# Optimization experiments

Measured on AMD Instinct MI355X. Metric: run time of the kernel, lower is better.

## Reference

```python
import jax, jax.numpy as jnp
import numpy as np
from jax import lax

N = 1024          # n_ligand == n_receptor == feature dim (required by broadcast in source)
D = 1024          # gnn_input_dim == gnn_output_dim
H = 32            # hopi_output_dim
C = 32            # cnn_channels


def setup_inputs() -> dict:
    key = jax.random.key(0)
    ks = jax.random.split(key, 24)
    s = 0.02
    inp = {
        "ligand_node_features": jax.random.normal(ks[0], (N, D), jnp.float32),
        "ligand_edge_features": jax.random.normal(ks[1], (N, D), jnp.float32),
        "ligand_adjacency": jax.random.uniform(ks[2], (N, N), jnp.float32),
        "receptor_node_features": jax.random.normal(ks[3], (N, D), jnp.float32),
        "receptor_edge_features": jax.random.normal(ks[4], (N, D), jnp.float32),
        "receptor_adjacency": jax.random.uniform(ks[5], (N, N), jnp.float32),
        # GNNLayer params (shared between ligand and receptor, as in source)
        "Wn": jax.random.normal(ks[6], (D, D), jnp.float32) * s,
        "bn": jax.random.normal(ks[7], (D,), jnp.float32) * s,
        "We": jax.random.normal(ks[8], (D, D), jnp.float32) * s,
        "be": jax.random.normal(ks[9], (D,), jnp.float32) * s,
        "Wa": jax.random.normal(ks[10], (1, D), jnp.float32) * s,
        "ba": jax.random.normal(ks[11], (1,), jnp.float32) * s,
        # HighOrderPairwiseInteraction: Linear(2*D -> H)
        "W_hopi": jax.random.normal(ks[12], (H, 2 * D), jnp.float32) * s,
        "b_hopi": jax.random.normal(ks[13], (H,), jnp.float32) * s,
        # CNN tail
        "conv1_w": jax.random.normal(ks[14], (C, H, 3, 3), jnp.float32) * s,
        "conv1_b": jax.random.normal(ks[15], (C,), jnp.float32) * s,
        "conv2_w": jax.random.normal(ks[16], (C, C, 3, 3), jnp.float32) * s,
        "conv2_b": jax.random.normal(ks[17], (C,), jnp.float32) * s,
        "conv3_w": jax.random.normal(ks[18], (1, C, 1, 1), jnp.float32) * s,
        "conv3_b": jax.random.normal(ks[19], (1,), jnp.float32) * s,
    }
    return inp


def _gnn(nf, ef, Wn, bn, We, be, Wa, ba):
    # aggregated: [N, D]
    agg = jnp.tanh(nf @ Wn.T + bn + ef @ We.T + be)
    scores = agg @ Wa.T + ba                      # [N, 1]
    attn = jax.nn.softmax(scores, axis=1)         # softmax over size-1 dim -> ones (faithful)
    weighted = jnp.sum(agg * attn, axis=1)        # [N]
    return nf + weighted                          # [N,D] + [N] broadcasts over last dim (D == N)


def _conv(x, w, b):
    y = lax.conv_general_dilated(x, w, (1, 1), "SAME",
                                 dimension_numbers=("NCHW", "OIHW", "NCHW"))
    return y + b[None, :, None, None]


def reference(ligand_node_features, ligand_edge_features, ligand_adjacency,
              receptor_node_features, receptor_edge_features, receptor_adjacency,
              Wn, bn, We, be, Wa, ba, W_hopi, b_hopi,
              conv1_w, conv1_b, conv2_w, conv2_b, conv3_w, conv3_b):
    lig = _gnn(ligand_node_features, ligand_edge_features, Wn, bn, We, be, Wa, ba)
    rec = _gnn(receptor_node_features, receptor_edge_features, Wn, bn, We, be, Wa, ba)

    # HOPI: interactions[i, j] = Linear(cat(lig[i], rec[j])) == lig[i] @ Wl.T + rec[j] @ Wr.T + b
    Wl, Wr = W_hopi[:, :D], W_hopi[:, D:]
    lig_p = lig @ Wl.T                            # [N, H]
    rec_p = rec @ Wr.T                            # [N, H]
    interactions = lig_p[:, None, :] + rec_p[None, :, :] + b_hopi  # [N, N, H]

    x = jnp.transpose(interactions, (2, 0, 1))[None]  # [1, H, N, N]
    x = jax.nn.relu(_conv(x, conv1_w, conv1_b))
    x = jax.nn.relu(_conv(x, conv2_w, conv2_b))
    x = _conv(x, conv3_w, conv3_b)                # [1, 1, N, N]
    return x[0, 0]                                # [N, N]
```

## Files before the change

### kernel.cpp

```cpp
#include <hip/hip_runtime.h>


typedef _Float16 half8 __attribute__((ext_vector_type(8)));
typedef _Float16 half4 __attribute__((ext_vector_type(4)));
typedef float    f32x4 __attribute__((ext_vector_type(4)));

__device__ __forceinline__ short f2h_bits(float f){
    _Float16 h = (_Float16)f;
    return __builtin_bit_cast(short, h);
}
__device__ __forceinline__ half8 pack2(const float4& x, const float4& y){
    half8 r;
    r[0] = (_Float16)x.x; r[1] = (_Float16)x.y;
    r[2] = (_Float16)x.z; r[3] = (_Float16)x.w;
    r[4] = (_Float16)y.x; r[5] = (_Float16)y.y;
    r[6] = (_Float16)y.z; r[7] = (_Float16)y.w;
    return r;
}
__device__ __forceinline__ half4 pack4(const float4& x){
    half4 r;
    r[0] = (_Float16)x.x; r[1] = (_Float16)x.y;
    r[2] = (_Float16)x.z; r[3] = (_Float16)x.w;
    return r;
}
__device__ __forceinline__ float tanh_fast(float x){
    float e = __expf(2.f * x);
    return 1.f - 2.f / (e + 1.f);
}

#define SWZ(c) ((((c) >> 1) & 3) << 3)

#define GNN_LOAD(AV, BV, KBN) {                                              \
    const int kbn_ = (KBN) & 2047;                                           \
    const float* Asrc_ = (kbn_ < 1024) ? A0 : A1;                            \
    const float* Bsrc_ = (kbn_ < 1024) ? Wn : We;                            \
    const int kk_ = kbn_ & 1023;                                             \
    const float* ap_ = Asrc_ + (size_t)(j0 + arow) * 1024 + kk_ + akc;       \
    const float* bp_ = Bsrc_ + (size_t)(d0 + brow) * 1024 + kk_ + bkc;       \
    AV[0] = *reinterpret_cast<const float4*>(ap_);                           \
    AV[1] = *reinterpret_cast<const float4*>(ap_ + 4);                       \
    AV[2] = *reinterpret_cast<const float4*>(ap_ + 8);                       \
    AV[3] = *reinterpret_cast<const float4*>(ap_ + 12);                      \
    BV[0] = *reinterpret_cast<const float4*>(bp_);                           \
    BV[1] = *reinterpret_cast<const float4*>(bp_ + 4);                       \
}

#define GNN_STAGE(AV, BV) {                                                  \
    const int ga_ = (t & 3) * 2;                                             \
    const int sa_ = arow & 7;                                                \
    *reinterpret_cast<half8*>(&As[arow * 64 + ((ga_    ) ^ sa_) * 8]) = pack2(AV[0], AV[1]); \
    *reinterpret_cast<half8*>(&As[arow * 64 + ((ga_ + 1) ^ sa_) * 8]) = pack2(AV[2], AV[3]); \
    *reinterpret_cast<half8*>(&Bs[brow * 64 + ((t & 7) ^ (brow & 7)) * 8]) = pack2(BV[0], BV[1]); \
}

#define GNN_MFMA() {                                                         \
    _Pragma("unroll")                                                        \
    for (int ks = 0; ks < 2; ++ks){                                          \
        half8 Af[2], Bf[2];                                                  \
        _Pragma("unroll")                                                    \
        for (int m = 0; m < 2; ++m){                                         \
            int row = wm * 32 + m * 16 + lr;                                 \
            int g   = ((ks * 4 + lg) ^ (row & 7)) * 8;                       \
            Af[m] = *reinterpret_cast<const half8*>(&As[row * 64 + g]);      \
        }                                                                    \
        _Pragma("unroll")                                                    \
        for (int n = 0; n < 2; ++n){                                         \
            int col = wn * 32 + n * 16 + lr;                                 \
            int g   = ((ks * 4 + lg) ^ (col & 7)) * 8;                       \
            Bf[n] = *reinterpret_cast<const half8*>(&Bs[col * 64 + g]);      \
        }                                                                    \
        _Pragma("unroll")                                                    \
        for (int m = 0; m < 2; ++m)                                          \
            _Pragma("unroll")                                                \
            for (int n = 0; n < 2; ++n)                                      \
                acc[m][n] = __builtin_amdgcn_mfma_f32_16x16x32_f16(          \
                    Af[m], Bf[n], acc[m][n], 0, 0, 0);                       \
    }                                                                        \
}

__global__ __launch_bounds__(512) void gnn_kernel(
    const float* __restrict__ lig_nf, const float* __restrict__ lig_ef,
    const float* __restrict__ rec_nf, const float* __restrict__ rec_ef,
    const float* __restrict__ Wn, const float* __restrict__ We,
    const float* __restrict__ bn, const float* __restrict__ be,
    float* __restrict__ part)
{
    __shared__ __attribute__((aligned(16))) short As[128 * 64];
    __shared__ __attribute__((aligned(16))) short Bs[64 * 64];
    __shared__ float red[128][2];

    const int t  = threadIdx.x;
    const int cx = blockIdx.z;
    const float* A0 = cx ? rec_nf : lig_nf;
    const float* A1 = cx ? rec_ef : lig_ef;
    const int j0 = blockIdx.x * 128;
    const int d0 = blockIdx.y * 64;

    const int wid  = t >> 6;
    const int wm   = wid >> 1;
    const int wn   = wid & 1;
    const int lane = t & 63;
    const int lr   = lane & 15;
    const int lg   = lane >> 4;

    f32x4 acc[2][2];
    #pragma unroll
    for (int m = 0; m < 2; ++m)
        #pragma unroll
        for (int n = 0; n < 2; ++n)
            acc[m][n] = (f32x4){0.f, 0.f, 0.f, 0.f};

    const int arow = t >> 2;
    const int akc  = (t & 3) * 16;
    const int brow = t >> 3;
    const int bkc  = (t & 7) * 8;

    float4 avA[4], bvA[2], avB[4], bvB[2];
    GNN_LOAD(avA, bvA, 0);
    GNN_LOAD(avB, bvB, 64);

    for (int kb = 0; kb < 2048; kb += 128){
        __syncthreads();
        GNN_STAGE(avA, bvA);
        GNN_LOAD(avA, bvA, kb + 128);
        __syncthreads();
        GNN_MFMA();
        __syncthreads();
        GNN_STAGE(avB, bvB);
        GNN_LOAD(avB, bvB, kb + 192);
        __syncthreads();
        GNN_MFMA();
    }

    float rowsum[2][4];
    #pragma unroll
    for (int m = 0; m < 2; ++m)
        #pragma unroll
        for (int jj = 0; jj < 4; ++jj) rowsum[m][jj] = 0.f;
    #pragma unroll
    for (int n = 0; n < 2; ++n){
        int d = d0 + wn * 32 + n * 16 + lr;
        float bias = bn[d] + be[d];
        #pragma unroll
        for (int m = 0; m < 2; ++m)
            #pragma unroll
            for (int jj = 0; jj < 4; ++jj)
                rowsum[m][jj] += tanh_fast(acc[m][n][jj] + bias);
    }
    #pragma unroll
    for (int mask = 1; mask < 16; mask <<= 1)
        #pragma unroll
        for (int m = 0; m < 2; ++m)
            #pragma unroll
            for (int jj = 0; jj < 4; ++jj)
                rowsum[m][jj] += __shfl_xor(rowsum[m][jj], mask);
    __syncthreads();
    if (lr == 0){
        #pragma unroll
        for (int m = 0; m < 2; ++m)
            #pragma unroll
            for (int jj = 0; jj < 4; ++jj)
                red[wm * 32 + m * 16 + lg * 4 + jj][wn] = rowsum[m][jj];
    }
    __syncthreads();
    if (t < 128)
        part[(size_t)cx * 16384 + (size_t)blockIdx.y * 1024 + j0 + t]
            = red[t][0] + red[t][1];
}

__global__ __launch_bounds__(512) void pp_kernel(
    const float* __restrict__ lig_nf, const float* __restrict__ rec_nf,
    const float* __restrict__ W_hopi, const float* __restrict__ b_hopi,
    const float* __restrict__ w1, const float* __restrict__ b1,
    const float* __restrict__ w2,
    const float* __restrict__ part,
    float* __restrict__ Kp, short* __restrict__ U16, short* __restrict__ V16,
    short* __restrict__ w2f16)
{
    __shared__ __attribute__((aligned(16))) char smem[47232];
    const int t = threadIdx.x;
    const int role = blockIdx.x;

    if (role < 32){
        short* Pz = reinterpret_cast<short*>(smem + 14336);
        short* Ws = reinterpret_cast<short*>(smem + 20736);

        const int cx = role >> 4;
        const int r0 = (role & 15) * 64;
        const float* nf = cx ? rec_nf : lig_nf;
        const float* W  = W_hopi + (cx ? 1024 : 0);
        short* O = cx ? V16 : U16;

        const int wid = t >> 6;
        const int lane = t & 63;
        const int lr = lane & 15;
        const int lg = lane >> 4;

        f32x4 pacc[2];
        pacc[0] = (f32x4){0.f, 0.f, 0.f, 0.f};
        pacc[1] = (f32x4){0.f, 0.f, 0.f, 0.f};

        if (wid < 5){
            const int lrow = wid * 16 + lr;
            const int grow = r0 - 8 + lrow;
            const bool ok = (unsigned)grow < 1024u;
            const float* ap = nf + (size_t)(ok ? grow : 0) * 1024 + lg * 8;
            const float* b0 = W + (size_t)lr * 2048 + lg * 8;
            const float* b1p = W + (size_t)(16 + lr) * 2048 + lg * 8;

            #pragma unroll 4
            for (int kb = 0; kb < 1024; kb += 32){
                float4 a0 = make_float4(0.f, 0.f, 0.f, 0.f);
                float4 a1 = a0;
                if (ok){
                    a0 = *reinterpret_cast<const float4*>(ap + kb);
                    a1 = *reinterpret_cast<const float4*>(ap + kb + 4);
                }
                half8 Af = pack2(a0, a1);
                half8 B0 = pack2(*reinterpret_cast<const float4*>(b0 + kb),
                                 *reinterpret_cast<const float4*>(b0 + kb + 4));
                half8 B1 = pack2(*reinterpret_cast<const float4*>(b1p + kb),
                                 *reinterpret_cast<const float4*>(b1p + kb + 4));
                pacc[0] = __builtin_amdgcn_mfma_f32_16x16x32_f16(Af, B0, pacc[0], 0, 0, 0);
                pacc[1] = __builtin_amdgcn_mfma_f32_16x16x32_f16(Af, B1, pacc[1], 0, 0, 0);
            }
            #pragma unroll
            for (int n = 0; n < 2; ++n)
                #pragma unroll
                for (int jj = 0; jj < 4; ++jj){
                    int rowl = wid * 16 + lg * 4 + jj;
                    Pz[rowl * 40 + n * 16 + lr] = f2h_bits(pacc[n][jj]);
                }
        }

        #pragma unroll
        for (int q = 0; q < 2; ++q){
            int pr = t * 2 + q;
            int co = pr >> 5;
            int ci = pr & 31;
            const float* wp = w1 + co * 288 + ci * 9;
            float tap[9];
            #pragma unroll
            for (int e = 0; e < 9; ++e) tap[e] = wp[e];
            #pragma unroll
            for (int d = 0; d < 3; ++d){
                float ta, tb, tc;
                if (cx == 0){ ta = tap[d * 3 + 0]; tb = tap[d * 3 + 1]; tc = tap[d * 3 + 2]; }
                else        { ta = tap[0 + d];     tb = tap[3 + d];     tc = tap[6 + d]; }
                Ws[(0 * 32 + co) * 104 + d * 32 + ci] = f2h_bits(ta + tb + tc);
                Ws[(1 * 32 + co) * 104 + d * 32 + ci] = f2h_bits(tb + tc);
                Ws[(2 * 32 + co) * 104 + d * 32 + ci] = f2h_bits(ta + tb);
            }
        }
        __syncthreads();

        if (wid < 4){
            f32x4 uacc[3][2];
            #pragma unroll
            for (int cs = 0; cs < 3; ++cs)
                #pragma unroll
                for (int n = 0; n < 2; ++n)
                    uacc[cs][n] = (f32x4){0.f, 0.f, 0.f, 0.f};
            #pragma unroll
            for (int d = 0; d < 3; ++d){
                int ar = wid * 16 + lr;
                half8 Ap = *reinterpret_cast<const half8*>(
                    &Pz[(7 + ar + d) * 40 + lg * 8]);
                #pragma unroll
                for (int cs = 0; cs < 3; ++cs)
                    #pragma unroll
                    for (int n = 0; n < 2; ++n){
                        half8 Bp = *reinterpret_cast<const half8*>(
                            &Ws[(cs * 32 + n * 16 + lr) * 104 + d * 32 + lg * 8]);
                        uacc[cs][n] = __builtin_amdgcn_mfma_f32_16x16x32_f16(
                            Ap, Bp, uacc[cs][n], 0, 0, 0);
                    }
            }
            #pragma unroll
            for (int cs = 0; cs < 3; ++cs)
                #pragma unroll
                for (int n = 0; n < 2; ++n)
                    #pragma unroll
                    for (int jj = 0; jj < 4; ++jj){
                        int grow = r0 + wid * 16 + lg * 4 + jj;
                        O[((size_t)(cs << 10) + grow) * 32 + n * 16 + lr]
                            = f2h_bits(uacc[cs][n][jj]);
                    }
        }
        return;
    }

    if (role == 33){
        #pragma unroll
        for (int q = 0; q < 18; ++q){
            int e = t + q * 512;
            int co  = e / 288;
            int rem = e - co * 288;
            int ci  = rem / 9;
            int tap = rem - ci * 9;
            w2f16[(tap * 32 + co) * 32 + (ci ^ SWZ(co))] = f2h_bits(w2[e]);
        }
        return;
    }

    float* ws_l = reinterpret_cast<float*>(smem);
    float* ws_r = reinterpret_cast<float*>(smem + 4096);
    float* red  = reinterpret_cast<float*>(smem + 8192);
    float* cvs  = reinterpret_cast<float*>(smem + 10240);
    float* w1s  = reinterpret_cast<float*>(smem + 10368);

    #pragma unroll
    for (int q = 0; q < 5; ++q){
        int i4 = t + q * 512;
        if (i4 < 2304)
            *reinterpret_cast<float4*>(&w1s[i4 * 4]) =
                *reinterpret_cast<const float4*>(w1 + i4 * 4);
    }
    for (int j = t; j < 1024; j += 512){
        float sl = 0.f, sr = 0.f;
        #pragma unroll
        for (int b = 0; b < 16; ++b){
            sl += part[b * 1024 + j];
            sr += part[16384 + b * 1024 + j];
        }
        ws_l[j] = sl; ws_r[j] = sr;
    }
    __syncthreads();
    {
        const int h = t & 31;
        const int seg = t >> 5;
        const float* wl = W_hopi + (size_t)h * 2048 + seg * 64;
        const float* wr = wl + 1024;
        float s = 0.f;
        #pragma unroll 8
        for (int j = 0; j < 64; j += 4){
            float4 a = *reinterpret_cast<const float4*>(wl + j);
            float4 b = *reinterpret_cast<const float4*>(wr + j);
            const float* l = &ws_l[seg * 64 + j];
            const float* r = &ws_r[seg * 64 + j];
            s = fmaf(l[0], a.x, s); s = fmaf(l[1], a.y, s);
            s = fmaf(l[2], a.z, s); s = fmaf(l[3], a.w, s);
            s = fmaf(r[0], b.x, s); s = fmaf(r[1], b.y, s);
            s = fmaf(r[2], b.z, s); s = fmaf(r[3], b.w, s);
        }
        red[t] = s;
    }
    __syncthreads();
    if (t < 32){
        float tot = b_hopi[t];
        #pragma unroll
        for (int g = 0; g < 16; ++g) tot += red[g * 32 + t];
        cvs[t] = tot;
    }
    __syncthreads();
    for (int e = t; e < 288; e += 512){
        int co  = e & 31;
        int cse = e >> 5;
        int yc  = cse / 3, xc = cse - yc * 3;
        float sum = b1[co];
        for (int ci = 0; ci < 32; ++ci){
            const float* wp = &w1s[co * 288 + ci * 9];
            float t00 = wp[0], t01 = wp[1], t02 = wp[2];
            float t10 = wp[3], t11 = wp[4], t12 = wp[5];
            float t20 = wp[6], t21 = wp[7], t22 = wp[8];
            float r0, r1, r2;
            if (xc == 0){ r0 = t00+t01+t02; r1 = t10+t11+t12; r2 = t20+t21+t22; }
            else if (xc == 1){ r0 = t01+t02; r1 = t11+t12; r2 = t21+t22; }
            else { r0 = t00+t01; r1 = t10+t11; r2 = t20+t21; }
            float wsum = (yc == 0) ? (r0+r1+r2) : ((yc == 1) ? (r1+r2) : (r0+r1));
            sum = fmaf(cvs[ci], wsum, sum);
        }
        Kp[cse * 32 + co] = sum;
    }
}

__global__ __launch_bounds__(512) void conv_kernel(
    const short* __restrict__ U16, const short* __restrict__ V16,
    const float* __restrict__ Kp, const short* __restrict__ w2f16,
    const float* __restrict__ b2,
    const float* __restrict__ w3, const float* __restrict__ b3,
    float* __restrict__ outp)
{
    __shared__ __attribute__((aligned(16))) short ys[18 * 18 * 32];
    __shared__ __attribute__((aligned(16))) short wB[9 * 32 * 32];

    const int t    = threadIdx.x;
    const int oy0  = blockIdx.y * 16;
    const int ox0  = blockIdx.x * 16;
    const int wid  = t >> 6;
    const int lane = t & 63;
    const int lr   = lane & 15;
    const int lg   = lane >> 4;

    {
        const uint4* src = reinterpret_cast<const uint4*>(w2f16);
        uint4* dst = reinterpret_cast<uint4*>(wB);
        #pragma unroll
        for (int e = t; e < 1152; e += 512)
            dst[e] = src[e];
    }
    const bool interior = (blockIdx.x >= 1) & (blockIdx.x <= 62) &
                          (blockIdx.y >= 1) & (blockIdx.y <= 62);
    if (interior){
        const int cp = (t & 7) * 4;
        half4 k00;
        {
            float4 kf = *reinterpret_cast<const float4*>(&Kp[cp]);
            k00[0] = (_Float16)kf.x; k00[1] = (_Float16)kf.y;
            k00[2] = (_Float16)kf.z; k00[3] = (_Float16)kf.w;
        }
        #pragma unroll
        for (int pass = 0; pass < 6; ++pass){
            int idx = t + pass * 512;
            if (idx < 2592){
                int po  = idx >> 3;
                int ryo = po / 18;
                int rxo = po - ryo * 18;
                int gy = oy0 - 1 + ryo, gx = ox0 - 1 + rxo;
                half4 u = *reinterpret_cast<const half4*>(&U16[gy * 32 + cp]);
                half4 v = *reinterpret_cast<const half4*>(&V16[gx * 32 + cp]);
                half4 r = u + v + k00;
                #pragma unroll
                for (int e = 0; e < 4; ++e)
                    r[e] = r[e] > (_Float16)0.f ? r[e] : (_Float16)0.f;
                *reinterpret_cast<half4*>(&ys[po * 32 + (cp ^ SWZ(rxo))]) = r;
            }
        }
    } else {
        #pragma unroll
        for (int pass = 0; pass < 6; ++pass){
            int idx = t + pass * 512;
            if (idx < 2592){
                int po  = idx >> 3;
                int cp  = (idx & 7) * 4;
                int ryo = po / 18;
                int rxo = po - ryo * 18;
                int gy = oy0 - 1 + ryo, gx = ox0 - 1 + rxo;
                half4 h = {(_Float16)0.f, (_Float16)0.f, (_Float16)0.f, (_Float16)0.f};
                if ((unsigned)gy < 1024u && (unsigned)gx < 1024u){
                    int yc = (gy == 0) ? 1 : ((gy == 1023) ? 2 : 0);
                    int xc = (gx == 0) ? 1 : ((gx == 1023) ? 2 : 0);
                    half4 u = *reinterpret_cast<const half4*>(
                        &U16[((size_t)(xc << 10) + gy) * 32 + cp]);
                    half4 v = *reinterpret_cast<const half4*>(
                        &V16[((size_t)(yc << 10) + gx) * 32 + cp]);
                    float4 k = *reinterpret_cast<const float4*>(&Kp[(yc * 3 + xc) * 32 + cp]);
                    h[0] = (_Float16)fmaxf((float)u[0] + (float)v[0] + k.x, 0.f);
                    h[1] = (_Float16)fmaxf((float)u[1] + (float)v[1] + k.y, 0.f);
                    h[2] = (_Float16)fmaxf((float)u[2] + (float)v[2] + k.z, 0.f);
                    h[3] = (_Float16)fmaxf((float)u[3] + (float)v[3] + k.w, 0.f);
                }
                *reinterpret_cast<half4*>(&ys[po * 32 + (cp ^ SWZ(rxo))]) = h;
            }
        }
    }
    __syncthreads();

    {
        half8 Bf[2][9];
        float bias[2], w3v[2];
        #pragma unroll
        for (int n = 0; n < 2; ++n){
            int co = n * 16 + lr;
            bias[n] = b2[co];
            w3v[n]  = w3[co];
            #pragma unroll
            for (int tap = 0; tap < 9; ++tap)
                Bf[n][tap] = *reinterpret_cast<const half8*>(
                    &wB[(tap * 32 + co) * 32 + ((lg * 8) ^ SWZ(co))]);
        }
        const float b3v = b3[0];
        for (int s = wid; s < 16; s += 8){
            int p  = s * 16 + lr;
            int ry = p >> 4;
            int rx = p & 15;
            f32x4 acc0 = {0.f, 0.f, 0.f, 0.f};
            f32x4 acc1 = {0.f, 0.f, 0.f, 0.f};
            #pragma unroll
            for (int tap = 0; tap < 9; ++tap){
                const int dy = tap / 3, dx = tap - (tap / 3) * 3;
                int pix = (ry + dy) * 18 + rx + dx;
                half8 A = *reinterpret_cast<const half8*>(
                    &ys[pix * 32 + ((lg * 8) ^ SWZ(rx + dx))]);
                acc0 = __builtin_amdgcn_mfma_f32_16x16x32_f16(A, Bf[0][tap], acc0, 0, 0, 0);
                acc1 = __builtin_amdgcn_mfma_f32_16x16x32_f16(A, Bf[1][tap], acc1, 0, 0, 0);
            }
            float part[4];
            #pragma unroll
            for (int j = 0; j < 4; ++j)
                part[j] = w3v[0] * fmaxf(acc0[j] + bias[0], 0.f)
                        + w3v[1] * fmaxf(acc1[j] + bias[1], 0.f);
            #pragma unroll
            for (int m = 1; m < 16; m <<= 1)
                #pragma unroll
                for (int j = 0; j < 4; ++j)
                    part[j] += __shfl_xor(part[j], m);
            if (lr == 0){
                float4 o = make_float4(part[0] + b3v, part[1] + b3v,
                                       part[2] + b3v, part[3] + b3v);
                *reinterpret_cast<float4*>(outp + (size_t)(oy0 + s) * 1024 + ox0 + lg * 4) = o;
            }
        }
    }
}

extern "C" void kernel_launch(void* const* d_in, const int* in_sizes, int n_in,
                              void* d_out, int out_size, void* d_ws, size_t ws_size,
                              hipStream_t stream)
{
    const float* lig_nf = (const float*)d_in[0];
    const float* lig_ef = (const float*)d_in[1];
    const float* rec_nf = (const float*)d_in[3];
    const float* rec_ef = (const float*)d_in[4];
    const float* Wn     = (const float*)d_in[6];
    const float* bn     = (const float*)d_in[7];
    const float* We     = (const float*)d_in[8];
    const float* be     = (const float*)d_in[9];
    const float* W_hopi = (const float*)d_in[12];
    const float* b_hopi = (const float*)d_in[13];
    const float* w1     = (const float*)d_in[14];
    const float* b1     = (const float*)d_in[15];
    const float* w2     = (const float*)d_in[16];
    const float* b2     = (const float*)d_in[17];
    const float* w3     = (const float*)d_in[18];
    const float* b3     = (const float*)d_in[19];
    float* outp = (float*)d_out;

    float* part  = (float*)d_ws;
    float* Kp    = (float*)((char*)d_ws + 393216);
    short* U16   = (short*)((char*)d_ws + 394368);
    short* V16   = (short*)((char*)d_ws + 590976);
    short* w2f16 = (short*)((char*)d_ws + 787584);

    dim3 g1(8, 16, 2);
    gnn_kernel<<<g1, 512, 0, stream>>>(lig_nf, lig_ef, rec_nf, rec_ef,
                                       Wn, We, bn, be, part);
    pp_kernel<<<34, 512, 0, stream>>>(lig_nf, rec_nf, W_hopi, b_hopi,
                                      w1, b1, w2, part, Kp, U16, V16, w2f16);
    dim3 g3(64, 64);
    conv_kernel<<<g3, 512, 0, stream>>>(U16, V16, Kp, w2f16, b2, w3, b3, outp);
}
```

Before: 114.2 us.

## Fuse HOPI projection of node features into GNN GEMM kernel blocks

The projection of node features onto W_hopi (nf @ W^T, 32 outputs) now runs inside the GNN GEMM kernel's blockIdx.y==0 blocks. Those blocks reuse the already-staged fp16 node-feature tiles from the first half of the K loop and write the result to a workspace buffer. The post-processing kernel then only loads the precomputed projections with halo rows instead of re-reading the 1024-wide node features with only 5 waves across 32 blocks. This removes a serial, poorly parallel GEMV-like phase from the small kernel. The cost is extra work and LDS in 16 of the GNN blocks, which may create load imbalance in that kernel.

```diff
diff --git a/kernel.cpp b/kernel.cpp
--- a/kernel.cpp
+++ b/kernel.cpp
@@ -51,6 +51,15 @@
     *reinterpret_cast<half8*>(&As[arow * 64 + ((ga_    ) ^ sa_) * 8]) = pack2(AV[0], AV[1]); \
     *reinterpret_cast<half8*>(&As[arow * 64 + ((ga_ + 1) ^ sa_) * 8]) = pack2(AV[2], AV[3]); \
     *reinterpret_cast<half8*>(&Bs[brow * 64 + ((t & 7) ^ (brow & 7)) * 8]) = pack2(BV[0], BV[1]); \
+}
+
+#define GNN_STAGE_W(KBS) {                                                   \
+    const int r32_ = t >> 4;                                                 \
+    const int kc_  = (t & 15) * 4;                                           \
+    float4 wv_ = *reinterpret_cast<const float4*>(                           \
+        Wp + (size_t)r32_ * 2048 + (KBS) + kc_);                             \
+    *reinterpret_cast<half4*>(                                               \
+        &Bs2[r32_ * 64 + ((((t & 15) >> 1)) ^ (r32_ & 7)) * 8 + (t & 1) * 4]) = pack4(wv_); \
 }
 
 #define GNN_MFMA() {                                                         \
@@ -78,23 +87,45 @@
     }                                                                        \
 }
 
+#define GNN_PMFMA() {                                                        \
+    _Pragma("unroll")                                                        \
+    for (int ks = 0; ks < 2; ++ks){                                          \
+        int prow = wid * 16 + lr;                                            \
+        half8 Af = *reinterpret_cast<const half8*>(                          \
+            &As[prow * 64 + ((ks * 4 + lg) ^ (prow & 7)) * 8]);              \
+        _Pragma("unroll")                                                    \
+        for (int n = 0; n < 2; ++n){                                         \
+            int col = n * 16 + lr;                                           \
+            half8 Bf2 = *reinterpret_cast<const half8*>(                     \
+                &Bs2[col * 64 + ((ks * 4 + lg) ^ (col & 7)) * 8]);           \
+            pacc[n] = __builtin_amdgcn_mfma_f32_16x16x32_f16(                \
+                Af, Bf2, pacc[n], 0, 0, 0);                                  \
+        }                                                                    \
+    }                                                                        \
+}
+
 __global__ __launch_bounds__(512) void gnn_kernel(
     const float* __restrict__ lig_nf, const float* __restrict__ lig_ef,
     const float* __restrict__ rec_nf, const float* __restrict__ rec_ef,
     const float* __restrict__ Wn, const float* __restrict__ We,
     const float* __restrict__ bn, const float* __restrict__ be,
-    float* __restrict__ part)
+    const float* __restrict__ W_hopi,
+    float* __restrict__ part,
+    short* __restrict__ Pw)
 {
     __shared__ __attribute__((aligned(16))) short As[128 * 64];
     __shared__ __attribute__((aligned(16))) short Bs[64 * 64];
+    __shared__ __attribute__((aligned(16))) short Bs2[32 * 64];
     __shared__ float red[128][2];
 
     const int t  = threadIdx.x;
     const int cx = blockIdx.z;
     const float* A0 = cx ? rec_nf : lig_nf;
     const float* A1 = cx ? rec_ef : lig_ef;
+    const float* Wp = W_hopi + (cx ? 1024 : 0);
     const int j0 = blockIdx.x * 128;
     const int d0 = blockIdx.y * 64;
+    const bool doP = (blockIdx.y == 0);
 
     const int wid  = t >> 6;
     const int wm   = wid >> 1;
@@ -109,6 +140,9 @@
         #pragma unroll
         for (int n = 0; n < 2; ++n)
             acc[m][n] = (f32x4){0.f, 0.f, 0.f, 0.f};
+    f32x4 pacc[2];
+    pacc[0] = (f32x4){0.f, 0.f, 0.f, 0.f};
+    pacc[1] = (f32x4){0.f, 0.f, 0.f, 0.f};
 
     const int arow = t >> 2;
     const int akc  = (t & 3) * 16;
@@ -120,16 +154,22 @@
     GNN_LOAD(avB, bvB, 64);
 
     for (int kb = 0; kb < 2048; kb += 128){
+        const bool pA = doP && (kb < 1024);
+        const bool pB = doP && (kb + 64 < 1024);
         __syncthreads();
         GNN_STAGE(avA, bvA);
+        if (pA) GNN_STAGE_W(kb);
         GNN_LOAD(avA, bvA, kb + 128);
         __syncthreads();
         GNN_MFMA();
+        if (pA) GNN_PMFMA();
         __syncthreads();
         GNN_STAGE(avB, bvB);
+        if (pB) GNN_STAGE_W(kb + 64);
         GNN_LOAD(avB, bvB, kb + 192);
         __syncthreads();
         GNN_MFMA();
+        if (pB) GNN_PMFMA();
     }
 
     float rowsum[2][4];
@@ -166,14 +206,24 @@
     if (t < 128)
         part[(size_t)cx * 16384 + (size_t)blockIdx.y * 1024 + j0 + t]
             = red[t][0] + red[t][1];
-}
-
-__global__ __launch_bounds__(512) void pp_kernel(
-    const float* __restrict__ lig_nf, const float* __restrict__ rec_nf,
+
+    if (doP){
+        #pragma unroll
+        for (int n = 0; n < 2; ++n)
+            #pragma unroll
+            for (int jj = 0; jj < 4; ++jj){
+                int grow = j0 + wid * 16 + lg * 4 + jj;
+                Pw[(size_t)cx * 32768 + (size_t)grow * 32 + n * 16 + lr]
+                    = f2h_bits(pacc[n][jj]);
+            }
+    }
+}
+
+__global__ __launch_bounds__(512) void pp2_kernel(
     const float* __restrict__ W_hopi, const float* __restrict__ b_hopi,
     const float* __restrict__ w1, const float* __restrict__ b1,
     const float* __restrict__ w2,
-    const float* __restrict__ part,
+    const float* __restrict__ part, const short* __restrict__ Pw,
     float* __restrict__ Kp, short* __restrict__ U16, short* __restrict__ V16,
     short* __restrict__ w2f16)
 {
@@ -182,55 +232,26 @@
     const int role = blockIdx.x;
 
     if (role < 32){
-        short* Pz = reinterpret_cast<short*>(smem + 14336);
-        short* Ws = reinterpret_cast<short*>(smem + 20736);
+        short* Pz = reinterpret_cast<short*>(smem);
+        short* Ws = reinterpret_cast<short*>(smem + 5376);
 
         const int cx = role >> 4;
         const int r0 = (role & 15) * 64;
-        const float* nf = cx ? rec_nf : lig_nf;
-        const float* W  = W_hopi + (cx ? 1024 : 0);
         short* O = cx ? V16 : U16;
+        const short* Psrc = Pw + (size_t)cx * 32768;
 
         const int wid = t >> 6;
         const int lane = t & 63;
         const int lr = lane & 15;
         const int lg = lane >> 4;
 
-        f32x4 pacc[2];
-        pacc[0] = (f32x4){0.f, 0.f, 0.f, 0.f};
-        pacc[1] = (f32x4){0.f, 0.f, 0.f, 0.f};
-
-        if (wid < 5){
-            const int lrow = wid * 16 + lr;
-            const int grow = r0 - 8 + lrow;
-            const bool ok = (unsigned)grow < 1024u;
-            const float* ap = nf + (size_t)(ok ? grow : 0) * 1024 + lg * 8;
-            const float* b0 = W + (size_t)lr * 2048 + lg * 8;
-            const float* b1p = W + (size_t)(16 + lr) * 2048 + lg * 8;
-
-            #pragma unroll 4
-            for (int kb = 0; kb < 1024; kb += 32){
-                float4 a0 = make_float4(0.f, 0.f, 0.f, 0.f);
-                float4 a1 = a0;
-                if (ok){
-                    a0 = *reinterpret_cast<const float4*>(ap + kb);
-                    a1 = *reinterpret_cast<const float4*>(ap + kb + 4);
-                }
-                half8 Af = pack2(a0, a1);
-                half8 B0 = pack2(*reinterpret_cast<const float4*>(b0 + kb),
-                                 *reinterpret_cast<const float4*>(b0 + kb + 4));
-                half8 B1 = pack2(*reinterpret_cast<const float4*>(b1p + kb),
-                                 *reinterpret_cast<const float4*>(b1p + kb + 4));
-                pacc[0] = __builtin_amdgcn_mfma_f32_16x16x32_f16(Af, B0, pacc[0], 0, 0, 0);
-                pacc[1] = __builtin_amdgcn_mfma_f32_16x16x32_f16(Af, B1, pacc[1], 0, 0, 0);
-            }
-            #pragma unroll
-            for (int n = 0; n < 2; ++n)
-                #pragma unroll
-                for (int jj = 0; jj < 4; ++jj){
-                    int rowl = wid * 16 + lg * 4 + jj;
-                    Pz[rowl * 40 + n * 16 + lr] = f2h_bits(pacc[n][jj]);
-                }
+        for (int idx = t; idx < 2112; idx += 512){
+            int l = idx >> 5;
+            int h = idx & 31;
+            int gr = r0 - 1 + l;
+            short v = 0;
+            if ((unsigned)gr < 1024u) v = Psrc[(size_t)gr * 32 + h];
+            Pz[l * 40 + h] = v;
         }
 
         #pragma unroll
@@ -265,7 +286,7 @@
             for (int d = 0; d < 3; ++d){
                 int ar = wid * 16 + lr;
                 half8 Ap = *reinterpret_cast<const half8*>(
-                    &Pz[(7 + ar + d) * 40 + lg * 8]);
+                    &Pz[(ar + d) * 40 + lg * 8]);
                 #pragma unroll
                 for (int cs = 0; cs < 3; ++cs)
                     #pragma unroll
@@ -527,6 +548,7 @@
     float* outp = (float*)d_out;
 
     float* part  = (float*)d_ws;
+    short* Pw    = (short*)((char*)d_ws + 131072);
     float* Kp    = (float*)((char*)d_ws + 393216);
     short* U16   = (short*)((char*)d_ws + 394368);
     short* V16   = (short*)((char*)d_ws + 590976);
@@ -534,9 +556,9 @@
 
     dim3 g1(8, 16, 2);
     gnn_kernel<<<g1, 512, 0, stream>>>(lig_nf, lig_ef, rec_nf, rec_ef,
-                                       Wn, We, bn, be, part);
-    pp_kernel<<<34, 512, 0, stream>>>(lig_nf, rec_nf, W_hopi, b_hopi,
-                                      w1, b1, w2, part, Kp, U16, V16, w2f16);
+                                       Wn, We, bn, be, W_hopi, part, Pw);
+    pp2_kernel<<<34, 512, 0, stream>>>(W_hopi, b_hopi, w1, b1, w2,
+                                       part, Pw, Kp, U16, V16, w2f16);
     dim3 g3(64, 64);
     conv_kernel<<<g3, 512, 0, stream>>>(U16, V16, Kp, w2f16, b2, w3, b3, outp);
 }
```

New measurement: 118.3 us. 1.04x slower.

## Split HOPI projection into a wide split-K kernel feeding a smaller post-processing kernel

Applied to the files above, without the earlier changes.

The HOPI projection (nf @ W_hopi slices) moves out of a 34-block kernel into a new 145-block kernel. Each block handles 16 rows, its 8 waves split K, and the partial sums are reduced in shared memory. The result is written as fp16 to the workspace. The constant-vector reduction is also spread across 16 blocks that write partial sums. A second kernel then loads the precomputed projections with halo rows and performs the conv1 collapse and the Kp computation. This removes the serial 1024-deep K loop and the redundant halo-row recomputation in only 32 blocks, in exchange for one extra kernel launch and a workspace round trip.

```diff
diff --git a/kernel.cpp b/kernel.cpp
--- a/kernel.cpp
+++ b/kernel.cpp
@@ -15,12 +15,6 @@
     r[2] = (_Float16)x.z; r[3] = (_Float16)x.w;
     r[4] = (_Float16)y.x; r[5] = (_Float16)y.y;
     r[6] = (_Float16)y.z; r[7] = (_Float16)y.w;
-    return r;
-}
-__device__ __forceinline__ half4 pack4(const float4& x){
-    half4 r;
-    r[0] = (_Float16)x.x; r[1] = (_Float16)x.y;
-    r[2] = (_Float16)x.z; r[3] = (_Float16)x.w;
     return r;
 }
 __device__ __forceinline__ float tanh_fast(float x){
@@ -168,69 +162,153 @@
             = red[t][0] + red[t][1];
 }
 
-__global__ __launch_bounds__(512) void pp_kernel(
+__global__ __launch_bounds__(512) void pk_kernel(
     const float* __restrict__ lig_nf, const float* __restrict__ rec_nf,
-    const float* __restrict__ W_hopi, const float* __restrict__ b_hopi,
+    const float* __restrict__ W_hopi, const float* __restrict__ w2,
+    const float* __restrict__ part,
+    short* __restrict__ Pw, float* __restrict__ cpart,
+    short* __restrict__ w2f16)
+{
+    __shared__ __attribute__((aligned(16))) char smem[16384];
+    const int t = threadIdx.x;
+    const int role = blockIdx.x;
+
+    if (role < 128){
+        float* red = reinterpret_cast<float*>(smem);
+        const int cx = role >> 6;
+        const int r0 = (role & 63) * 16;
+        const float* nf = cx ? rec_nf : lig_nf;
+        const float* W  = W_hopi + (cx ? 1024 : 0);
+
+        const int wid = t >> 6;
+        const int lane = t & 63;
+        const int lr = lane & 15;
+        const int lg = lane >> 4;
+
+        f32x4 pacc[2];
+        pacc[0] = (f32x4){0.f, 0.f, 0.f, 0.f};
+        pacc[1] = (f32x4){0.f, 0.f, 0.f, 0.f};
+
+        const float* ap  = nf + (size_t)(r0 + lr) * 1024 + lg * 8;
+        const float* b0  = W + (size_t)lr * 2048 + lg * 8;
+        const float* b1p = W + (size_t)(16 + lr) * 2048 + lg * 8;
+        const int kbase = wid * 128;
+
+        #pragma unroll
+        for (int ks = 0; ks < 4; ++ks){
+            const int kb = kbase + ks * 32;
+            half8 Af = pack2(*reinterpret_cast<const float4*>(ap + kb),
+                             *reinterpret_cast<const float4*>(ap + kb + 4));
+            half8 B0 = pack2(*reinterpret_cast<const float4*>(b0 + kb),
+                             *reinterpret_cast<const float4*>(b0 + kb + 4));
+            half8 B1 = pack2(*reinterpret_cast<const float4*>(b1p + kb),
+                             *reinterpret_cast<const float4*>(b1p + kb + 4));
+            pacc[0] = __builtin_amdgcn_mfma_f32_16x16x32_f16(Af, B0, pacc[0], 0, 0, 0);
+            pacc[1] = __builtin_amdgcn_mfma_f32_16x16x32_f16(Af, B1, pacc[1], 0, 0, 0);
+        }
+        #pragma unroll
+        for (int n = 0; n < 2; ++n)
+            #pragma unroll
+            for (int jj = 0; jj < 4; ++jj)
+                red[(wid * 16 + lg * 4 + jj) * 32 + n * 16 + lr] = pacc[n][jj];
+        __syncthreads();
+        {
+            const int row = t >> 5;
+            const int h   = t & 31;
+            float s = 0.f;
+            #pragma unroll
+            for (int w = 0; w < 8; ++w)
+                s += red[(w * 16 + row) * 32 + h];
+            Pw[(size_t)cx * 32768 + (size_t)(r0 + row) * 32 + h] = f2h_bits(s);
+        }
+        return;
+    }
+
+    if (role == 144){
+        #pragma unroll
+        for (int q = 0; q < 18; ++q){
+            int e = t + q * 512;
+            int co  = e / 288;
+            int rem = e - co * 288;
+            int ci  = rem / 9;
+            int tap = rem - ci * 9;
+            w2f16[(tap * 32 + co) * 32 + (ci ^ SWZ(co))] = f2h_bits(w2[e]);
+        }
+        return;
+    }
+
+    {
+        float* ws_l = reinterpret_cast<float*>(smem);
+        float* ws_r = reinterpret_cast<float*>(smem + 256);
+        float* red  = reinterpret_cast<float*>(smem + 512);
+
+        const int q  = role - 128;
+        const int jb = q * 64;
+
+        if (t < 64){
+            int j = jb + t;
+            float sl = 0.f, sr = 0.f;
+            #pragma unroll
+            for (int b = 0; b < 16; ++b){
+                sl += part[b * 1024 + j];
+                sr += part[16384 + b * 1024 + j];
+            }
+            ws_l[t] = sl; ws_r[t] = sr;
+        }
+        __syncthreads();
+
+        const int h = t >> 4;
+        const int g = t & 15;
+        const float* wl = W_hopi + (size_t)h * 2048 + jb + g * 4;
+        const float* wr = wl + 1024;
+        float4 a = *reinterpret_cast<const float4*>(wl);
+        float4 b = *reinterpret_cast<const float4*>(wr);
+        const float* l = &ws_l[g * 4];
+        const float* r = &ws_r[g * 4];
+        float s = l[0] * a.x + l[1] * a.y + l[2] * a.z + l[3] * a.w
+                + r[0] * b.x + r[1] * b.y + r[2] * b.z + r[3] * b.w;
+        red[t] = s;
+        __syncthreads();
+        if (t < 32){
+            float tot = 0.f;
+            #pragma unroll
+            for (int gg = 0; gg < 16; ++gg) tot += red[t * 16 + gg];
+            cpart[q * 32 + t] = tot;
+        }
+    }
+}
+
+__global__ __launch_bounds__(512) void pp2_kernel(
+    const float* __restrict__ b_hopi,
     const float* __restrict__ w1, const float* __restrict__ b1,
-    const float* __restrict__ w2,
-    const float* __restrict__ part,
-    float* __restrict__ Kp, short* __restrict__ U16, short* __restrict__ V16,
-    short* __restrict__ w2f16)
+    const short* __restrict__ Pw, const float* __restrict__ cpart,
+    float* __restrict__ Kp, short* __restrict__ U16, short* __restrict__ V16)
 {
     __shared__ __attribute__((aligned(16))) char smem[47232];
     const int t = threadIdx.x;
     const int role = blockIdx.x;
 
     if (role < 32){
-        short* Pz = reinterpret_cast<short*>(smem + 14336);
-        short* Ws = reinterpret_cast<short*>(smem + 20736);
+        short* Pz = reinterpret_cast<short*>(smem);
+        short* Ws = reinterpret_cast<short*>(smem + 5376);
 
         const int cx = role >> 4;
         const int r0 = (role & 15) * 64;
-        const float* nf = cx ? rec_nf : lig_nf;
-        const float* W  = W_hopi + (cx ? 1024 : 0);
         short* O = cx ? V16 : U16;
+        const short* Psrc = Pw + (size_t)cx * 32768;
 
         const int wid = t >> 6;
         const int lane = t & 63;
         const int lr = lane & 15;
         const int lg = lane >> 4;
 
-        f32x4 pacc[2];
-        pacc[0] = (f32x4){0.f, 0.f, 0.f, 0.f};
-        pacc[1] = (f32x4){0.f, 0.f, 0.f, 0.f};
-
-        if (wid < 5){
-            const int lrow = wid * 16 + lr;
-            const int grow = r0 - 8 + lrow;
-            const bool ok = (unsigned)grow < 1024u;
-            const float* ap = nf + (size_t)(ok ? grow : 0) * 1024 + lg * 8;
-            const float* b0 = W + (size_t)lr * 2048 + lg * 8;
-            const float* b1p = W + (size_t)(16 + lr) * 2048 + lg * 8;
-
-            #pragma unroll 4
-            for (int kb = 0; kb < 1024; kb += 32){
-                float4 a0 = make_float4(0.f, 0.f, 0.f, 0.f);
-                float4 a1 = a0;
-                if (ok){
-                    a0 = *reinterpret_cast<const float4*>(ap + kb);
-                    a1 = *reinterpret_cast<const float4*>(ap + kb + 4);
-                }
-                half8 Af = pack2(a0, a1);
-                half8 B0 = pack2(*reinterpret_cast<const float4*>(b0 + kb),
-                                 *reinterpret_cast<const float4*>(b0 + kb + 4));
-                half8 B1 = pack2(*reinterpret_cast<const float4*>(b1p + kb),
-                                 *reinterpret_cast<const float4*>(b1p + kb + 4));
-                pacc[0] = __builtin_amdgcn_mfma_f32_16x16x32_f16(Af, B0, pacc[0], 0, 0, 0);
-                pacc[1] = __builtin_amdgcn_mfma_f32_16x16x32_f16(Af, B1, pacc[1], 0, 0, 0);
-            }
-            #pragma unroll
-            for (int n = 0; n < 2; ++n)
-                #pragma unroll
-                for (int jj = 0; jj < 4; ++jj){
-                    int rowl = wid * 16 + lg * 4 + jj;
-                    Pz[rowl * 40 + n * 16 + lr] = f2h_bits(pacc[n][jj]);
-                }
+        for (int idx = t; idx < 2112; idx += 512){
+            int l = idx >> 5;
+            int h = idx & 31;
+            int gr = r0 - 1 + l;
+            short v = 0;
+            if ((unsigned)gr < 1024u) v = Psrc[(size_t)gr * 32 + h];
+            Pz[l * 40 + h] = v;
         }
 
         #pragma unroll
@@ -265,7 +343,7 @@
             for (int d = 0; d < 3; ++d){
                 int ar = wid * 16 + lr;
                 half8 Ap = *reinterpret_cast<const half8*>(
-                    &Pz[(7 + ar + d) * 40 + lg * 8]);
+                    &Pz[(ar + d) * 40 + lg * 8]);
                 #pragma unroll
                 for (int cs = 0; cs < 3; ++cs)
                     #pragma unroll
@@ -290,87 +368,43 @@
         return;
     }
 
-    if (role == 33){
-        #pragma unroll
-        for (int q = 0; q < 18; ++q){
-            int e = t + q * 512;
-            int co  = e / 288;
-            int rem = e - co * 288;
-            int ci  = rem / 9;
-            int tap = rem - ci * 9;
-            w2f16[(tap * 32 + co) * 32 + (ci ^ SWZ(co))] = f2h_bits(w2[e]);
-        }
-        return;
-    }
-
-    float* ws_l = reinterpret_cast<float*>(smem);
-    float* ws_r = reinterpret_cast<float*>(smem + 4096);
-    float* red  = reinterpret_cast<float*>(smem + 8192);
-    float* cvs  = reinterpret_cast<float*>(smem + 10240);
-    float* w1s  = reinterpret_cast<float*>(smem + 10368);
-
-    #pragma unroll
-    for (int q = 0; q < 5; ++q){
-        int i4 = t + q * 512;
-        if (i4 < 2304)
-            *reinterpret_cast<float4*>(&w1s[i4 * 4]) =
-                *reinterpret_cast<const float4*>(w1 + i4 * 4);
-    }
-    for (int j = t; j < 1024; j += 512){
-        float sl = 0.f, sr = 0.f;
-        #pragma unroll
-        for (int b = 0; b < 16; ++b){
-            sl += part[b * 1024 + j];
-            sr += part[16384 + b * 1024 + j];
-        }
-        ws_l[j] = sl; ws_r[j] = sr;
-    }
-    __syncthreads();
     {
-        const int h = t & 31;
-        const int seg = t >> 5;
-        const float* wl = W_hopi + (size_t)h * 2048 + seg * 64;
-        const float* wr = wl + 1024;
-        float s = 0.f;
-        #pragma unroll 8
-        for (int j = 0; j < 64; j += 4){
-            float4 a = *reinterpret_cast<const float4*>(wl + j);
-            float4 b = *reinterpret_cast<const float4*>(wr + j);
-            const float* l = &ws_l[seg * 64 + j];
-            const float* r = &ws_r[seg * 64 + j];
-            s = fmaf(l[0], a.x, s); s = fmaf(l[1], a.y, s);
-            s = fmaf(l[2], a.z, s); s = fmaf(l[3], a.w, s);
-            s = fmaf(r[0], b.x, s); s = fmaf(r[1], b.y, s);
-            s = fmaf(r[2], b.z, s); s = fmaf(r[3], b.w, s);
-        }
-        red[t] = s;
-    }
-    __syncthreads();
-    if (t < 32){
-        float tot = b_hopi[t];
-        #pragma unroll
-        for (int g = 0; g < 16; ++g) tot += red[g * 32 + t];
-        cvs[t] = tot;
-    }
-    __syncthreads();
-    for (int e = t; e < 288; e += 512){
-        int co  = e & 31;
-        int cse = e >> 5;
-        int yc  = cse / 3, xc = cse - yc * 3;
-        float sum = b1[co];
-        for (int ci = 0; ci < 32; ++ci){
-            const float* wp = &w1s[co * 288 + ci * 9];
-            float t00 = wp[0], t01 = wp[1], t02 = wp[2];
-            float t10 = wp[3], t11 = wp[4], t12 = wp[5];
-            float t20 = wp[6], t21 = wp[7], t22 = wp[8];
-            float r0, r1, r2;
-            if (xc == 0){ r0 = t00+t01+t02; r1 = t10+t11+t12; r2 = t20+t21+t22; }
-            else if (xc == 1){ r0 = t01+t02; r1 = t11+t12; r2 = t21+t22; }
-            else { r0 = t00+t01; r1 = t10+t11; r2 = t20+t21; }
-            float wsum = (yc == 0) ? (r0+r1+r2) : ((yc == 1) ? (r1+r2) : (r0+r1));
-            sum = fmaf(cvs[ci], wsum, sum);
-        }
-        Kp[cse * 32 + co] = sum;
+        float* cvs = reinterpret_cast<float*>(smem);
+        float* w1s = reinterpret_cast<float*>(smem + 128);
+
+        #pragma unroll
+        for (int q = 0; q < 5; ++q){
+            int i4 = t + q * 512;
+            if (i4 < 2304)
+                *reinterpret_cast<float4*>(&w1s[i4 * 4]) =
+                    *reinterpret_cast<const float4*>(w1 + i4 * 4);
+        }
+        if (t < 32){
+            float tot = b_hopi[t];
+            #pragma unroll
+            for (int q = 0; q < 16; ++q) tot += cpart[q * 32 + t];
+            cvs[t] = tot;
+        }
+        __syncthreads();
+        for (int e = t; e < 288; e += 512){
+            int co  = e & 31;
+            int cse = e >> 5;
+            int yc  = cse / 3, xc = cse - yc * 3;
+            float sum = b1[co];
+            for (int ci = 0; ci < 32; ++ci){
+                const float* wp = &w1s[co * 288 + ci * 9];
+                float t00 = wp[0], t01 = wp[1], t02 = wp[2];
+                float t10 = wp[3], t11 = wp[4], t12 = wp[5];
+                float t20 = wp[6], t21 = wp[7], t22 = wp[8];
+                float r0v, r1v, r2v;
+                if (xc == 0){ r0v = t00+t01+t02; r1v = t10+t11+t12; r2v = t20+t21+t22; }
+                else if (xc == 1){ r0v = t01+t02; r1v = t11+t12; r2v = t21+t22; }
+                else { r0v = t00+t01; r1v = t10+t11; r2v = t20+t21; }
+                float wsum = (yc == 0) ? (r0v+r1v+r2v) : ((yc == 1) ? (r1v+r2v) : (r0v+r1v));
+                sum = fmaf(cvs[ci], wsum, sum);
+            }
+            Kp[cse * 32 + co] = sum;
+        }
     }
 }
 
@@ -527,6 +561,8 @@
     float* outp = (float*)d_out;
 
     float* part  = (float*)d_ws;
+    short* Pw    = (short*)((char*)d_ws + 131072);
+    float* cpart = (float*)((char*)d_ws + 262144);
     float* Kp    = (float*)((char*)d_ws + 393216);
     short* U16   = (short*)((char*)d_ws + 394368);
     short* V16   = (short*)((char*)d_ws + 590976);
@@ -535,8 +571,10 @@
     dim3 g1(8, 16, 2);
     gnn_kernel<<<g1, 512, 0, stream>>>(lig_nf, lig_ef, rec_nf, rec_ef,
                                        Wn, We, bn, be, part);
-    pp_kernel<<<34, 512, 0, stream>>>(lig_nf, rec_nf, W_hopi, b_hopi,
-                                      w1, b1, w2, part, Kp, U16, V16, w2f16);
+    pk_kernel<<<145, 512, 0, stream>>>(lig_nf, rec_nf, W_hopi, w2,
+                                       part, Pw, cpart, w2f16);
+    pp2_kernel<<<33, 512, 0, stream>>>(b_hopi, w1, b1, Pw, cpart,
+                                       Kp, U16, V16);
     dim3 g3(64, 64);
     conv_kernel<<<g3, 512, 0, stream>>>(U16, V16, Kp, w2f16, b2, w3, b3, outp);
 }
```

Result: faster. 111.6 us (-2.2%).
